# Performance work log

Measured on AMD Instinct MI355X. Metric: run time of the kernel, lower is better.

The kernel has to match this reference:

```python
import jax, jax.numpy as jnp
import numpy as np

ALPHA = 0.2  # LeakyReLU negative slope
NEG_INF = -9e15


def setup_inputs() -> dict:
    key = jax.random.key(0)
    k1, k2, k3, k4 = jax.random.split(key, 4)
    N, F_in, F_out = 8192, 128, 64
    x = jax.random.normal(k1, (N, F_in), dtype=jnp.float32)
    adj = jax.random.randint(k2, (N, N), 0, 2, dtype=jnp.int32)
    W = jax.random.normal(k3, (F_in, F_out), dtype=jnp.float32) * 0.1
    a = jax.random.normal(k4, (2 * F_out, 1), dtype=jnp.float32) * 0.1
    return {"x": x, "adj": adj, "W": W, "a": a}


def reference(x, adj, W, a):
    F_out = W.shape[1]
    Wh = x @ W                         # [N, F_out]
    Wh1 = Wh @ a[:F_out, :]            # [N, 1]
    Wh2 = Wh @ a[F_out:, :]            # [N, 1]
    e = Wh1 + Wh2.T                    # [N, N] broadcast scores
    e = jnp.where(e > 0, e, ALPHA * e) # LeakyReLU
    e = jnp.where(adj > 0, e, NEG_INF) # mask non-edges
    attention = jax.nn.softmax(e, axis=1)
    out = attention @ Wh               # [N, F_out]
    return jax.nn.elu(out)             # concat=True -> ELU
```

## Files before the change

### kernel.cpp

```cpp
#include <hip/hip_runtime.h>
#include <hip/hip_bf16.h>

#define NN 8192
#define FIN 128
#define FOUT 64
#define ALPHA 0.2f
#define CHUNK 256
#define BM 16
#define NCHUNK (NN / CHUNK)
#define PROW (CHUNK + 8)

typedef __attribute__((ext_vector_type(8))) short short8;
typedef __attribute__((ext_vector_type(4))) float floatx4;

static __device__ __forceinline__ ushort f2bf(float f) {
    __hip_bfloat16 h = __float2bfloat16(f);
    return __builtin_bit_cast(ushort, h);
}

__global__ __launch_bounds__(256) void gat_proj(const float* __restrict__ x,
                                                const float* __restrict__ W,
                                                const float* __restrict__ a,
                                                ushort* __restrict__ WhT,
                                                float* __restrict__ Wh1,
                                                float* __restrict__ Wh2) {
    const int t = threadIdx.x;
    const int f = t & 63;
    const int rl = t >> 6;
    const int row = blockIdx.x * 4 + rl;
    const float4* __restrict__ x4 = (const float4*)(x + (size_t)row * FIN);

    float acc = 0.f;
    #pragma unroll
    for (int k4 = 0; k4 < FIN / 4; ++k4) {
        float4 xv = x4[k4];
        const int k = k4 * 4;
        acc = fmaf(xv.x, W[(k + 0) * FOUT + f], acc);
        acc = fmaf(xv.y, W[(k + 1) * FOUT + f], acc);
        acc = fmaf(xv.z, W[(k + 2) * FOUT + f], acc);
        acc = fmaf(xv.w, W[(k + 3) * FOUT + f], acc);
    }
    WhT[(size_t)f * NN + row] = f2bf(acc);

    float s1 = acc * a[f];
    float s2 = acc * a[FOUT + f];
    #pragma unroll
    for (int off = 32; off; off >>= 1) {
        s1 += __shfl_xor(s1, off, 64);
        s2 += __shfl_xor(s2, off, 64);
    }
    if (f == 0) { Wh1[row] = s1; Wh2[row] = s2; }
}

__global__ __launch_bounds__(256) void gat_attn(const int* __restrict__ adj,
                                                const ushort* __restrict__ WhT,
                                                const float* __restrict__ Wh1,
                                                const float* __restrict__ Wh2,
                                                float* __restrict__ out) {
    __shared__ __align__(16) ushort P[2][BM][PROW];
    __shared__ float denL[BM];

    const int t = threadIdx.x;
    const int lane = t & 63;
    const int wv = t >> 6;
    const int row0 = blockIdx.x * BM;
    const int ln = lane & 15;
    const int quad = lane >> 4;

    const float4 wh1v = *(const float4*)(Wh1 + row0 + wv * 4);
    const int* __restrict__ aptr = adj + (size_t)(row0 + wv * 4) * NN + lane * 4;

    floatx4 acc = {0.f, 0.f, 0.f, 0.f};
    float den0 = 0.f, den1 = 0.f, den2 = 0.f, den3 = 0.f;

    auto computeP = [&](int c, int b) {
        const int jb = c * CHUNK;
        const float4 wh2v = *(const float4*)(Wh2 + jb + lane * 4);
        const int4 av0 = *(const int4*)(aptr + (size_t)0 * NN + jb);
        const int4 av1 = *(const int4*)(aptr + (size_t)1 * NN + jb);
        const int4 av2 = *(const int4*)(aptr + (size_t)2 * NN + jb);
        const int4 av3 = *(const int4*)(aptr + (size_t)3 * NN + jb);
#define ROWP(AV, W1, DEN, II)                                              \
        {                                                                  \
            float s0 = (W1) + wh2v.x, s1 = (W1) + wh2v.y,                  \
                  s2 = (W1) + wh2v.z, s3 = (W1) + wh2v.w;                  \
            s0 = fmaxf(s0, ALPHA * s0); s1 = fmaxf(s1, ALPHA * s1);        \
            s2 = fmaxf(s2, ALPHA * s2); s3 = fmaxf(s3, ALPHA * s3);        \
            float p0 = __expf(s0), p1 = __expf(s1),                        \
                  p2 = __expf(s2), p3 = __expf(s3);                        \
            p0 = (AV.x > 0) ? p0 : 0.f; p1 = (AV.y > 0) ? p1 : 0.f;        \
            p2 = (AV.z > 0) ? p2 : 0.f; p3 = (AV.w > 0) ? p3 : 0.f;       \
            DEN += (p0 + p1) + (p2 + p3);                                  \
            ushort4 pk = make_ushort4(f2bf(p0), f2bf(p1), f2bf(p2), f2bf(p3)); \
            *(ushort4*)&P[b][wv * 4 + (II)][lane * 4] = pk;                \
        }
        ROWP(av0, wh1v.x, den0, 0)
        ROWP(av1, wh1v.y, den1, 1)
        ROWP(av2, wh1v.z, den2, 2)
        ROWP(av3, wh1v.w, den3, 3)
#undef ROWP
    };

    computeP(0, 0);
    __syncthreads();

    int pb = 0;
    for (int c = 0; c < NCHUNK; ++c) {
        if (c + 1 < NCHUNK) computeP(c + 1, pb ^ 1);

        const int jb = c * CHUNK;
        const ushort* Arow = &P[pb][ln][quad * 8];
        const ushort* Brow = WhT + (size_t)(wv * 16 + ln) * NN + jb + quad * 8;
        #pragma unroll
        for (int k0 = 0; k0 < 8; ++k0) {
            short8 af = *(const short8*)(Arow + k0 * 32);
            short8 bf = *(const short8*)(Brow + k0 * 32);
            acc = __builtin_amdgcn_mfma_f32_16x16x32_bf16(af, bf, acc, 0, 0, 0);
        }
        __syncthreads();
        pb ^= 1;
    }

    float dsum[4] = {den0, den1, den2, den3};
    #pragma unroll
    for (int ii = 0; ii < 4; ++ii) {
        float d = dsum[ii];
        #pragma unroll
        for (int off = 32; off; off >>= 1) d += __shfl_xor(d, off, 64);
        if (lane == 0) denL[wv * 4 + ii] = d;
    }
    __syncthreads();

    #pragma unroll
    for (int r = 0; r < 4; ++r) {
        const int i = quad * 4 + r;
        float o = acc[r] / denL[i];
        o = (o > 0.f) ? o : (__expf(o) - 1.f);
        out[(size_t)(row0 + i) * FOUT + wv * 16 + ln] = o;
    }
}

extern "C" void kernel_launch(void* const* d_in, const int* in_sizes, int n_in,
                              void* d_out, int out_size, void* d_ws, size_t ws_size,
                              hipStream_t stream) {
    const float* x   = (const float*)d_in[0];
    const int*   adj = (const int*)  d_in[1];
    const float* W   = (const float*)d_in[2];
    const float* a   = (const float*)d_in[3];
    float* out = (float*)d_out;

    ushort* WhT = (ushort*)d_ws;
    float* Wh1 = (float*)(WhT + (size_t)FOUT * NN);
    float* Wh2 = Wh1 + NN;

    gat_proj<<<NN / 4, 256, 0, stream>>>(x, W, a, WhT, Wh1, Wh2);
    gat_attn<<<NN / BM, 256, 0, stream>>>(adj, WhT, Wh1, Wh2, out);
}
```

Before: 398.2 us.

## Split attention over column slices with a combine pass, and coalesce WhT writes

The attention kernel is split along the neighbour dimension into four slices, so the grid has four times as many blocks. Each slice writes a partial numerator and denominator to workspace, and a new combine kernel sums them and applies the normalisation and ELU. The projection kernel now handles 32 rows per block and stages results in shared memory, so the transposed bf16 WhT writes are coalesced instead of strided. The cost is an extra kernel launch and about 8 MB of partial-sum traffic, traded for more parallelism over the 256 MB adjacency stream.

```diff
diff --git a/kernel.cpp b/kernel.cpp
--- a/kernel.cpp
+++ b/kernel.cpp
@@ -7,7 +7,9 @@
 #define ALPHA 0.2f
 #define CHUNK 256
 #define BM 16
-#define NCHUNK (NN / CHUNK)
+#define SPLIT 4
+#define JSLICE (NN / SPLIT)
+#define NCHUNK (JSLICE / CHUNK)
 #define PROW (CHUNK + 8)
 
 typedef __attribute__((ext_vector_type(8))) short short8;
@@ -24,58 +26,75 @@
                                                 ushort* __restrict__ WhT,
                                                 float* __restrict__ Wh1,
                                                 float* __restrict__ Wh2) {
+    __shared__ float tile[32][FOUT + 1];
+
     const int t = threadIdx.x;
     const int f = t & 63;
-    const int rl = t >> 6;
-    const int row = blockIdx.x * 4 + rl;
-    const float4* __restrict__ x4 = (const float4*)(x + (size_t)row * FIN);
+    const int wv = t >> 6;
+    const int row0 = blockIdx.x * 32;
+    const float af1 = a[f], af2 = a[FOUT + f];
 
-    float acc = 0.f;
+    for (int r8 = 0; r8 < 8; ++r8) {
+        const int row = row0 + wv * 8 + r8;
+        const float4* __restrict__ x4 = (const float4*)(x + (size_t)row * FIN);
+        float acc = 0.f;
+        #pragma unroll
+        for (int k4 = 0; k4 < FIN / 4; ++k4) {
+            float4 xv = x4[k4];
+            const int k = k4 * 4;
+            acc = fmaf(xv.x, W[(k + 0) * FOUT + f], acc);
+            acc = fmaf(xv.y, W[(k + 1) * FOUT + f], acc);
+            acc = fmaf(xv.z, W[(k + 2) * FOUT + f], acc);
+            acc = fmaf(xv.w, W[(k + 3) * FOUT + f], acc);
+        }
+        tile[wv * 8 + r8][f] = acc;
+
+        float s1 = acc * af1;
+        float s2 = acc * af2;
+        #pragma unroll
+        for (int off = 32; off; off >>= 1) {
+            s1 += __shfl_xor(s1, off, 64);
+            s2 += __shfl_xor(s2, off, 64);
+        }
+        if (f == 0) { Wh1[row] = s1; Wh2[row] = s2; }
+    }
+    __syncthreads();
+
+    const int r = t & 31;
+    const int fh = t >> 5;
     #pragma unroll
-    for (int k4 = 0; k4 < FIN / 4; ++k4) {
-        float4 xv = x4[k4];
-        const int k = k4 * 4;
-        acc = fmaf(xv.x, W[(k + 0) * FOUT + f], acc);
-        acc = fmaf(xv.y, W[(k + 1) * FOUT + f], acc);
-        acc = fmaf(xv.z, W[(k + 2) * FOUT + f], acc);
-        acc = fmaf(xv.w, W[(k + 3) * FOUT + f], acc);
+    for (int p = 0; p < 8; ++p) {
+        const int ff = p * 8 + fh;
+        WhT[(size_t)ff * NN + row0 + r] = f2bf(tile[r][ff]);
     }
-    WhT[(size_t)f * NN + row] = f2bf(acc);
-
-    float s1 = acc * a[f];
-    float s2 = acc * a[FOUT + f];
-    #pragma unroll
-    for (int off = 32; off; off >>= 1) {
-        s1 += __shfl_xor(s1, off, 64);
-        s2 += __shfl_xor(s2, off, 64);
-    }
-    if (f == 0) { Wh1[row] = s1; Wh2[row] = s2; }
 }
 
-__global__ __launch_bounds__(256) void gat_attn(const int* __restrict__ adj,
-                                                const ushort* __restrict__ WhT,
-                                                const float* __restrict__ Wh1,
-                                                const float* __restrict__ Wh2,
-                                                float* __restrict__ out) {
+__global__ __launch_bounds__(256) void gat_attn_part(const int* __restrict__ adj,
+                                                     const ushort* __restrict__ WhT,
+                                                     const float* __restrict__ Wh1,
+                                                     const float* __restrict__ Wh2,
+                                                     float* __restrict__ pnum,
+                                                     float* __restrict__ pden) {
     __shared__ __align__(16) ushort P[2][BM][PROW];
-    __shared__ float denL[BM];
 
     const int t = threadIdx.x;
     const int lane = t & 63;
     const int wv = t >> 6;
-    const int row0 = blockIdx.x * BM;
+    const int slice = blockIdx.x & (SPLIT - 1);
+    const int row0 = (blockIdx.x >> 2) * BM;
+    const int j0 = slice * JSLICE;
     const int ln = lane & 15;
     const int quad = lane >> 4;
 
     const float4 wh1v = *(const float4*)(Wh1 + row0 + wv * 4);
-    const int* __restrict__ aptr = adj + (size_t)(row0 + wv * 4) * NN + lane * 4;
+    const int* __restrict__ aptr = adj + (size_t)(row0 + wv * 4) * NN + j0 + lane * 4;
 
     floatx4 acc = {0.f, 0.f, 0.f, 0.f};
     float den0 = 0.f, den1 = 0.f, den2 = 0.f, den3 = 0.f;
 
     auto computeP = [&](int c, int b) {
         const int jb = c * CHUNK;
-        const float4 wh2v = *(const float4*)(Wh2 + jb + lane * 4);
+        const float4 wh2v = *(const float4*)(Wh2 + j0 + jb + lane * 4);
         const int4 av0 = *(const int4*)(aptr + (size_t)0 * NN + jb);
         const int4 av1 = *(const int4*)(aptr + (size_t)1 * NN + jb);
         const int4 av2 = *(const int4*)(aptr + (size_t)2 * NN + jb);
@@ -108,14 +127,14 @@
     for (int c = 0; c < NCHUNK; ++c) {
         if (c + 1 < NCHUNK) computeP(c + 1, pb ^ 1);
 
-        const int jb = c * CHUNK;
+        const int jb = j0 + c * CHUNK;
         const ushort* Arow = &P[pb][ln][quad * 8];
         const ushort* Brow = WhT + (size_t)(wv * 16 + ln) * NN + jb + quad * 8;
         #pragma unroll
         for (int k0 = 0; k0 < 8; ++k0) {
-            short8 af = *(const short8*)(Arow + k0 * 32);
-            short8 bf = *(const short8*)(Brow + k0 * 32);
-            acc = __builtin_amdgcn_mfma_f32_16x16x32_bf16(af, bf, acc, 0, 0, 0);
+            short8 afr = *(const short8*)(Arow + k0 * 32);
+            short8 bfr = *(const short8*)(Brow + k0 * 32);
+            acc = __builtin_amdgcn_mfma_f32_16x16x32_bf16(afr, bfr, acc, 0, 0, 0);
         }
         __syncthreads();
         pb ^= 1;
@@ -127,17 +146,30 @@
         float d = dsum[ii];
         #pragma unroll
         for (int off = 32; off; off >>= 1) d += __shfl_xor(d, off, 64);
-        if (lane == 0) denL[wv * 4 + ii] = d;
+        if (lane == 0) pden[(size_t)slice * NN + row0 + wv * 4 + ii] = d;
     }
-    __syncthreads();
 
     #pragma unroll
     for (int r = 0; r < 4; ++r) {
         const int i = quad * 4 + r;
-        float o = acc[r] / denL[i];
-        o = (o > 0.f) ? o : (__expf(o) - 1.f);
-        out[(size_t)(row0 + i) * FOUT + wv * 16 + ln] = o;
+        pnum[((size_t)slice * NN + row0 + i) * FOUT + wv * 16 + ln] = acc[r];
     }
+}
+
+__global__ __launch_bounds__(256) void gat_combine(const float* __restrict__ pnum,
+                                                   const float* __restrict__ pden,
+                                                   float* __restrict__ out) {
+    const int idx = blockIdx.x * 256 + threadIdx.x;
+    const int row = idx >> 6;
+    float num = 0.f, den = 0.f;
+    #pragma unroll
+    for (int s = 0; s < SPLIT; ++s) {
+        num += pnum[(size_t)s * NN * FOUT + idx];
+        den += pden[(size_t)s * NN + row];
+    }
+    float o = num / den;
+    o = (o > 0.f) ? o : (__expf(o) - 1.f);
+    out[idx] = o;
 }
 
 extern "C" void kernel_launch(void* const* d_in, const int* in_sizes, int n_in,
@@ -152,7 +184,10 @@
     ushort* WhT = (ushort*)d_ws;
     float* Wh1 = (float*)(WhT + (size_t)FOUT * NN);
     float* Wh2 = Wh1 + NN;
+    float* pnum = Wh2 + NN;
+    float* pden = pnum + (size_t)SPLIT * NN * FOUT;
 
-    gat_proj<<<NN / 4, 256, 0, stream>>>(x, W, a, WhT, Wh1, Wh2);
-    gat_attn<<<NN / BM, 256, 0, stream>>>(adj, WhT, Wh1, Wh2, out);
+    gat_proj<<<NN / 32, 256, 0, stream>>>(x, W, a, WhT, Wh1, Wh2);
+    gat_attn_part<<<(NN / BM) * SPLIT, 256, 0, stream>>>(adj, WhT, Wh1, Wh2, pnum, pden);
+    gat_combine<<<NN * FOUT / 256, 256, 0, stream>>>(pnum, pden, out);
 }
```

Result: no change. 398.7 us (+0.1%).
